# Kernel optimization log

Measured on AMD Instinct MI355X. Metric: run time of the kernel, lower is better.

The kernel has to match this reference:

```python
import jax, jax.numpy as jnp
import numpy as np

B, T, D, H, O = 64, 512, 64, 512, 64

def setup_inputs() -> dict:
    key = jax.random.key(0)
    ks = jax.random.split(key, 12)
    s = lambda fan: 1.0 / np.sqrt(fan)
    return {
        "x": jax.random.normal(ks[0], (B, T, D), jnp.float32),
        "W_ih0": jax.random.normal(ks[1], (4 * H, D), jnp.float32) * s(D),
        "W_hh0": jax.random.normal(ks[2], (4 * H, H), jnp.float32) * s(H),
        "b_ih0": jax.random.normal(ks[3], (4 * H,), jnp.float32) * s(H),
        "b_hh0": jax.random.normal(ks[4], (4 * H,), jnp.float32) * s(H),
        "W_ih1": jax.random.normal(ks[5], (4 * H, H), jnp.float32) * s(H),
        "W_hh1": jax.random.normal(ks[6], (4 * H, H), jnp.float32) * s(H),
        "b_ih1": jax.random.normal(ks[7], (4 * H,), jnp.float32) * s(H),
        "b_hh1": jax.random.normal(ks[8], (4 * H,), jnp.float32) * s(H),
        "lin_w": jax.random.normal(ks[9], (O, H), jnp.float32) * s(H),
        "lin_b": jax.random.normal(ks[10], (O,), jnp.float32) * s(H),
    }

def _lstm_layer(x_seq, h0, c0, W_ih, W_hh, b_ih, b_hh):
    # Precompute input contribution for all timesteps: [B, T, 4H]
    xg = jnp.einsum('btd,gd->btg', x_seq, W_ih) + b_ih
    def step(carry, xg_t):
        h, c = carry
        gates = xg_t + h @ W_hh.T + b_hh  # [B, 4H]
        i, f, g, o = jnp.split(gates, 4, axis=-1)
        i = jax.nn.sigmoid(i); f = jax.nn.sigmoid(f)
        g = jnp.tanh(g); o = jax.nn.sigmoid(o)
        c = f * c + i * g  # eval mode: dropout mask is identity
        h = o * jnp.tanh(c)
        return (h, c), h
    (h, c), ys = jax.lax.scan(step, (h0, c0), jnp.swapaxes(xg, 0, 1))
    return jnp.swapaxes(ys, 0, 1), h, c

def reference(x, W_ih0, W_hh0, b_ih0, b_hh0, W_ih1, W_hh1, b_ih1, b_hh1, lin_w, lin_b):
    h = jnp.zeros((x.shape[0], H), x.dtype)
    c = jnp.zeros((x.shape[0], H), x.dtype)
    # NOTE: faithful to source — h/c are only zeroed before layer 0 and
    # carried into layer 1 as its initial state.
    y0, h, c = _lstm_layer(x, h, c, W_ih0, W_hh0, b_ih0, b_hh0)
    y1, h, c = _lstm_layer(y0, h, c, W_ih1, W_hh1, b_ih1, b_hh1)
    return h @ lin_w.T + lin_b  # [B, O]
```

## Files before the change

kernel.cpp:

```cpp
#include <hip/hip_runtime.h>

#define TSEQ 512

typedef unsigned short us8v __attribute__((ext_vector_type(8)));
typedef __bf16 bf16x8 __attribute__((ext_vector_type(8)));
typedef float f32x4 __attribute__((ext_vector_type(4)));
typedef unsigned u32x4 __attribute__((ext_vector_type(4)));

#define OFF_FLAGS 0u
#define OFF_BIAS  524288u
#define OFF_X16   540672u
#define OFF_W0    4734976u
#define OFF_W1    7094272u
#define OFF_Y0    11288576u
#define OFF_RING  44843008u

static __device__ __forceinline__ unsigned short f2bf(float f) {
    unsigned u = __builtin_bit_cast(unsigned, f);
    u += 0x7fffu + ((u >> 16) & 1u);
    return (unsigned short)(u >> 16);
}
static __device__ __forceinline__ float sigmf(float x) { return 1.0f / (1.0f + __expf(-x)); }
static __device__ __forceinline__ float tanh_fast(float x) {
    float a = fabsf(x);
    float e = __expf(-2.0f * a);
    float t = (1.0f - e) / (1.0f + e);
    return copysignf(t, x);
}
static __device__ __forceinline__ f32x4 mfma16(us8v a, us8v b, f32x4 c) {
    return __builtin_amdgcn_mfma_f32_16x16x32_bf16(
        __builtin_bit_cast(bf16x8, a), __builtin_bit_cast(bf16x8, b), c, 0, 0, 0);
}

__global__ void setup_kernel(const float* __restrict__ x,
                             const float* __restrict__ wih0, const float* __restrict__ whh0,
                             const float* __restrict__ bih0, const float* __restrict__ bhh0,
                             const float* __restrict__ wih1, const float* __restrict__ whh1,
                             const float* __restrict__ bih1, const float* __restrict__ bhh1,
                             char* __restrict__ ws)
{
    unsigned idx = blockIdx.x * blockDim.x + threadIdx.x;
    unsigned stride = gridDim.x * blockDim.x;
    unsigned short* x16 = (unsigned short*)(ws + OFF_X16);
    unsigned short* w0  = (unsigned short*)(ws + OFF_W0);
    unsigned short* w1  = (unsigned short*)(ws + OFF_W1);
    float* bias = (float*)(ws + OFF_BIAS);
    const unsigned NX  = 64u*512u*64u;
    const unsigned NW0 = 2048u*576u;
    const unsigned NW1 = 2048u*1024u;
    const unsigned NT  = NX + NW0 + NW1 + 4096u;
    for (unsigned i = idx; i < NT; i += stride) {
        if (i < NX) {
            unsigned d = i & 63u, b = (i >> 6) & 63u, t = i >> 12;
            x16[i] = f2bf(x[((b << 9) + t) * 64u + d]);
        } else if (i < NX + NW0) {
            unsigned k = i - NX; unsigned r = k / 576u, c = k % 576u;
            float v = (c < 64u) ? wih0[r*64u + c] : whh0[r*512u + (c - 64u)];
            w0[k] = f2bf(v);
        } else if (i < NX + NW0 + NW1) {
            unsigned k = i - NX - NW0; unsigned r = k >> 10, c = k & 1023u;
            float v = (c < 512u) ? wih1[(r<<9) + c] : whh1[(r<<9) + (c - 512u)];
            w1[k] = f2bf(v);
        } else {
            unsigned k = i - NX - NW0 - NW1;
            float v = (k < 2048u) ? (bih0[k] + bhh0[k]) : (bih1[k-2048u] + bhh1[k-2048u]);
            bias[k] = v;
        }
    }
}

__launch_bounds__(256, 1)
__global__ void lstm_persist(char* __restrict__ ws)
{
    const int tid  = threadIdx.x;
    const int kq   = tid >> 6;
    const int lane = tid & 63;
    const int l15  = lane & 15;
    const int lhi  = lane >> 4;
    const int bg   = blockIdx.x & 3;
    const int hg   = blockIdx.x >> 2;

    unsigned* flags   = (unsigned*)(ws + OFF_FLAGS);
    const float* bias = (const float*)(ws + OFF_BIAS);
    const char*  x16  = ws + OFF_X16;
    char* y0   = ws + OFF_Y0;
    char* ring = ws + OFF_RING;

    __shared__ float gsum[64 * 68];
    __shared__ float bias_l[64];

    if (tid < 64) bias_l[tid] = bias[(tid >> 4)*512 + hg*16 + (tid & 15)];

    float cst = 0.0f;

    us8v A[4][8];
    {
        const char* w0p = ws + OFF_W0;
        #pragma unroll
        for (int m = 0; m < 4; ++m) {
            const char* base = w0p + (size_t)(m*512 + hg*16 + l15)*1152 + lhi*16;
            #pragma unroll
            for (int kk = 0; kk < 4; ++kk)
                A[m][kk] = *(const us8v*)(base + (2 + kq*4 + kk)*64);
            if (kq < 2) A[m][4] = *(const us8v*)(base + kq*64);
        }
    }
    __syncthreads();

    const int fragoff = l15*1024 + kq*256 + lhi*16;

#define POLL(WIDX) do {                                                              \
        const unsigned* fp_ = flags + (size_t)(WIDX)*128 + bg*32 + (lane & 31);      \
        unsigned fv_;                                                                \
        do {                                                                         \
            asm volatile("global_load_dword %0, %1, off sc0 sc1\n\ts_waitcnt vmcnt(0)" \
                         : "=v"(fv_) : "v"(fp_) : "memory");                         \
        } while (!__all(fv_ != 0u));                                                 \
    } while (0)

#define ACTIVATION_STORE(DSTBASE) do {                                               \
        int b_ = tid >> 4, p_ = tid & 15;                                            \
        float g4_[4];                                                                \
        _Pragma("unroll")                                                            \
        for (int g = 0; g < 4; ++g) {                                                \
            float s_ = bias_l[g*16 + p_];                                            \
            _Pragma("unroll")                                                        \
            for (int kk = 0; kk < 4; ++kk) s_ += gsum[(g*16 + p_)*68 + kk*17 + b_];  \
            g4_[g] = s_;                                                             \
        }                                                                            \
        float iv_ = sigmf(g4_[0]), fv_ = sigmf(g4_[1]);                              \
        float gv_ = tanh_fast(g4_[2]), ov_ = sigmf(g4_[3]);                          \
        cst = fv_*cst + iv_*gv_;                                                     \
        float h_ = ov_ * tanh_fast(cst);                                             \
        unsigned hv_ = f2bf(h_);                                                     \
        unsigned pk_ = (hv_ & 0xffffu) | (((unsigned)__shfl_xor((int)hv_, 1)) << 16);\
        if (!(p_ & 1)) {                                                             \
            const char* dst_ = (DSTBASE) + b_*1024 + (hg*16 + p_)*2;                 \
            asm volatile("global_store_dword %0, %1, off sc0 sc1"                    \
                         :: "v"(dst_), "v"(pk_) : "memory");                         \
        }                                                                            \
    } while (0)

    for (int t = 0; t < TSEQ; ++t) {
        us8v xf = {};
        if (kq < 2)
            xf = *(const us8v*)(x16 + (size_t)t*8192 + (bg*16 + l15)*128 + kq*64 + lhi*16);

        f32x4 acc[4] = {{0.f,0.f,0.f,0.f},{0.f,0.f,0.f,0.f},{0.f,0.f,0.f,0.f},{0.f,0.f,0.f,0.f}};
        if (t > 0) {
            POLL(t-1);
            const char* hb = y0 + ((size_t)(t-1)*4 + bg)*16384 + fragoff;
            us8v hf0 = *(const us8v*)(hb);
            us8v hf1 = *(const us8v*)(hb + 64);
            us8v hf2 = *(const us8v*)(hb + 128);
            us8v hf3 = *(const us8v*)(hb + 192);
            if (kq < 2) {
                #pragma unroll
                for (int m = 0; m < 4; ++m) acc[m] = mfma16(A[m][4], xf, acc[m]);
            }
            #pragma unroll
            for (int m = 0; m < 4; ++m) acc[m] = mfma16(A[m][0], hf0, acc[m]);
            #pragma unroll
            for (int m = 0; m < 4; ++m) acc[m] = mfma16(A[m][1], hf1, acc[m]);
            #pragma unroll
            for (int m = 0; m < 4; ++m) acc[m] = mfma16(A[m][2], hf2, acc[m]);
            #pragma unroll
            for (int m = 0; m < 4; ++m) acc[m] = mfma16(A[m][3], hf3, acc[m]);
        } else if (kq < 2) {
            #pragma unroll
            for (int m = 0; m < 4; ++m) acc[m] = mfma16(A[m][4], xf, acc[m]);
        }
        #pragma unroll
        for (int m = 0; m < 4; ++m) {
            #pragma unroll
            for (int q = 0; q < 4; ++q)
                gsum[(m*16 + lhi*4 + q)*68 + kq*17 + l15] = acc[m][q];
        }
        __syncthreads();
        ACTIVATION_STORE(y0 + ((size_t)t*4 + bg)*16384);
        asm volatile("s_waitcnt vmcnt(0)" ::: "memory");
        __syncthreads();
        if (tid == 0) {
            unsigned one = 1;
            const unsigned* fq = flags + (size_t)t*128 + bg*32 + hg;
            asm volatile("global_store_dword %0, %1, off sc0 sc1"
                         :: "v"(fq), "v"(one) : "memory");
        }
    }

    {
        const char* w1p = ws + OFF_W1;
        #pragma unroll
        for (int m = 0; m < 4; ++m) {
            const char* base = w1p + (size_t)(m*512 + hg*16 + l15)*2048 + lhi*16;
            #pragma unroll
            for (int kk = 0; kk < 4; ++kk) {
                A[m][kk]     = *(const us8v*)(base + (kq*4 + kk)*64);
                A[m][kk + 4] = *(const us8v*)(base + (16 + kq*4 + kk)*64);
            }
        }
    }
    if (tid < 64) bias_l[tid] = bias[2048 + (tid >> 4)*512 + hg*16 + (tid & 15)];
    __syncthreads();

    for (int t = 0; t < TSEQ; ++t) {
        const char* yb = y0 + ((size_t)t*4 + bg)*16384 + fragoff;
        us8v yf0 = *(const us8v*)(yb);
        us8v yf1 = *(const us8v*)(yb + 64);
        us8v yf2 = *(const us8v*)(yb + 128);
        us8v yf3 = *(const us8v*)(yb + 192);

        POLL(t == 0 ? 511 : 511 + t);

        const char* s1 = ((t == 0) ? (y0 + ((size_t)511*4 + bg)*16384)
                                   : (ring + ((size_t)((t-1) & 1)*4 + bg)*16384)) + fragoff;
        u32x4 r0, r1, r2, r3;
        {
            const char* a0 = s1;
            const char* a1 = s1 + 64;
            const char* a2 = s1 + 128;
            const char* a3 = s1 + 192;
            asm volatile("global_load_dwordx4 %0, %1, off sc0 sc1"
                         : "=v"(r0) : "v"(a0) : "memory");
            asm volatile("global_load_dwordx4 %0, %1, off sc0 sc1"
                         : "=v"(r1) : "v"(a1) : "memory");
            asm volatile("global_load_dwordx4 %0, %1, off sc0 sc1"
                         : "=v"(r2) : "v"(a2) : "memory");
            asm volatile("global_load_dwordx4 %0, %1, off sc0 sc1"
                         : "=v"(r3) : "v"(a3) : "memory");
        }

        f32x4 acc[4] = {{0.f,0.f,0.f,0.f},{0.f,0.f,0.f,0.f},{0.f,0.f,0.f,0.f},{0.f,0.f,0.f,0.f}};
        #pragma unroll
        for (int m = 0; m < 4; ++m) acc[m] = mfma16(A[m][0], yf0, acc[m]);
        #pragma unroll
        for (int m = 0; m < 4; ++m) acc[m] = mfma16(A[m][1], yf1, acc[m]);
        #pragma unroll
        for (int m = 0; m < 4; ++m) acc[m] = mfma16(A[m][2], yf2, acc[m]);
        #pragma unroll
        for (int m = 0; m < 4; ++m) acc[m] = mfma16(A[m][3], yf3, acc[m]);

        asm volatile("s_waitcnt vmcnt(0)"
                     : "+v"(r0), "+v"(r1), "+v"(r2), "+v"(r3) :: "memory");
        __builtin_amdgcn_sched_barrier(0);

        #pragma unroll
        for (int m = 0; m < 4; ++m) acc[m] = mfma16(A[m][4], __builtin_bit_cast(us8v, r0), acc[m]);
        #pragma unroll
        for (int m = 0; m < 4; ++m) acc[m] = mfma16(A[m][5], __builtin_bit_cast(us8v, r1), acc[m]);
        #pragma unroll
        for (int m = 0; m < 4; ++m) acc[m] = mfma16(A[m][6], __builtin_bit_cast(us8v, r2), acc[m]);
        #pragma unroll
        for (int m = 0; m < 4; ++m) acc[m] = mfma16(A[m][7], __builtin_bit_cast(us8v, r3), acc[m]);

        #pragma unroll
        for (int m = 0; m < 4; ++m) {
            #pragma unroll
            for (int q = 0; q < 4; ++q)
                gsum[(m*16 + lhi*4 + q)*68 + kq*17 + l15] = acc[m][q];
        }
        __syncthreads();
        ACTIVATION_STORE(ring + ((size_t)(t & 1)*4 + bg)*16384);
        asm volatile("s_waitcnt vmcnt(0)" ::: "memory");
        __syncthreads();
        if (tid == 0) {
            unsigned one = 1;
            const unsigned* fq = flags + (size_t)(512 + t)*128 + bg*32 + hg;
            asm volatile("global_store_dword %0, %1, off sc0 sc1"
                         :: "v"(fq), "v"(one) : "memory");
        }
    }
#undef POLL
#undef ACTIVATION_STORE
}

__global__ void final_linear(const char* __restrict__ ws,
                             const float* __restrict__ linw, const float* __restrict__ linb,
                             float* __restrict__ out)
{
    __shared__ float hrow[512];
    int b = blockIdx.x;
    int o = threadIdx.x;
    int bg = b >> 4, bl = b & 15;
    const char* src = ws + OFF_RING + ((size_t)1*4 + bg)*16384 + (size_t)bl*1024;
    {
        us8v v = *(const us8v*)(src + o*16);
        #pragma unroll
        for (int p = 0; p < 8; ++p)
            hrow[o*8+p] = __builtin_bit_cast(float, ((unsigned)v[p]) << 16);
    }
    __syncthreads();
    float acc = linb[o];
    const float* wrow = linw + o*512;
    #pragma unroll 8
    for (int k = 0; k < 512; ++k) acc += hrow[k] * wrow[k];
    out[b*64 + o] = acc;
}

extern "C" void kernel_launch(void* const* d_in, const int* in_sizes, int n_in,
                              void* d_out, int out_size, void* d_ws, size_t ws_size,
                              hipStream_t stream)
{
    const float* x    = (const float*)d_in[0];
    const float* wih0 = (const float*)d_in[1];
    const float* whh0 = (const float*)d_in[2];
    const float* bih0 = (const float*)d_in[3];
    const float* bhh0 = (const float*)d_in[4];
    const float* wih1 = (const float*)d_in[5];
    const float* whh1 = (const float*)d_in[6];
    const float* bih1 = (const float*)d_in[7];
    const float* bhh1 = (const float*)d_in[8];
    const float* linw = (const float*)d_in[9];
    const float* linb = (const float*)d_in[10];
    char* ws = (char*)d_ws;

    (void)hipMemsetAsync(ws + OFF_FLAGS, 0, 524288, stream);
    hipLaunchKernelGGL(setup_kernel, dim3(1024), dim3(256), 0, stream,
                       x, wih0, whh0, bih0, bhh0, wih1, whh1, bih1, bhh1, ws);
    hipLaunchKernelGGL(lstm_persist, dim3(128), dim3(256), 0, stream, ws);
    hipLaunchKernelGGL(final_linear, dim3(64), dim3(64), 0, stream,
                       ws, linw, linb, (float*)d_out);
}
```

Before: 2.603 ms.

## Replace per-step flag array with epoch counters and remove second block barrier

Per-step flag words are replaced by one epoch counter per workgroup, padded to its own 128-byte line. Consumers poll with a pipelined two-load asm loop that checks for epoch >= t. The trailing __syncthreads plus tid==0 flag store becomes an LDS atomic wave counter, so the last wave to finish publishes the epoch, and gsum is double-buffered so the next step can start without a second barrier. The hidden-state layout is also changed so each workgroup writes one contiguous 512-byte slice, with fragment loads adjusted to match. This cuts barrier and cross-workgroup signalling latency on the recurrent critical path, at the cost of subtler memory-ordering assumptions.

```diff
diff --git a/kernel.cpp b/kernel.cpp
--- a/kernel.cpp
+++ b/kernel.cpp
@@ -8,12 +8,12 @@
 typedef unsigned u32x4 __attribute__((ext_vector_type(4)));
 
 #define OFF_FLAGS 0u
-#define OFF_BIAS  524288u
-#define OFF_X16   540672u
-#define OFF_W0    4734976u
-#define OFF_W1    7094272u
-#define OFF_Y0    11288576u
-#define OFF_RING  44843008u
+#define OFF_BIAS  16384u
+#define OFF_X16   32768u
+#define OFF_W0    4227072u
+#define OFF_W1    6586368u
+#define OFF_Y0    10780672u
+#define OFF_RING  44335104u
 
 static __device__ __forceinline__ unsigned short f2bf(float f) {
     unsigned u = __builtin_bit_cast(unsigned, f);
@@ -31,6 +31,7 @@
     return __builtin_amdgcn_mfma_f32_16x16x32_bf16(
         __builtin_bit_cast(bf16x8, a), __builtin_bit_cast(bf16x8, b), c, 0, 0, 0);
 }
+static __device__ __forceinline__ us8v asb(u32x4 v) { return __builtin_bit_cast(us8v, v); }
 
 __global__ void setup_kernel(const float* __restrict__ x,
                              const float* __restrict__ wih0, const float* __restrict__ whh0,
@@ -80,15 +81,19 @@
     const int bg   = blockIdx.x & 3;
     const int hg   = blockIdx.x >> 2;
 
-    unsigned* flags   = (unsigned*)(ws + OFF_FLAGS);
     const float* bias = (const float*)(ws + OFF_BIAS);
     const char*  x16  = ws + OFF_X16;
     char* y0   = ws + OFF_Y0;
     char* ring = ws + OFF_RING;
-
-    __shared__ float gsum[64 * 68];
-    __shared__ float bias_l[64];
-
+    const char* flagbase = ws + OFF_FLAGS + bg*4096;
+    const char* fq       = flagbase + hg*128;
+
+    __shared__ __align__(16) char arena[86016];
+    float* gsum       = (float*)arena;
+    float* bias_l     = (float*)(arena + 34816);
+    unsigned* wcnt    = (unsigned*)(arena + 35072);
+
+    if (tid == 0) { wcnt[0] = 0u; wcnt[1] = 0u; }
     if (tid < 64) bias_l[tid] = bias[(tid >> 4)*512 + hg*16 + (tid & 15)];
 
     float cst = 0.0f;
@@ -107,85 +112,118 @@
     }
     __syncthreads();
 
-    const int fragoff = l15*1024 + kq*256 + lhi*16;
-
-#define POLL(WIDX) do {                                                              \
-        const unsigned* fp_ = flags + (size_t)(WIDX)*128 + bg*32 + (lane & 31);      \
-        unsigned fv_;                                                                \
-        do {                                                                         \
-            asm volatile("global_load_dword %0, %1, off sc0 sc1\n\ts_waitcnt vmcnt(0)" \
-                         : "=v"(fv_) : "v"(fp_) : "memory");                         \
-        } while (!__all(fv_ != 0u));                                                 \
+    const int base_off = kq*4096 + (lhi >> 1)*512 + l15*32 + (lhi & 1)*16;
+
+    unsigned pf0 = 0, pf1 = 0;
+
+#define POLL(EP) do {                                                            \
+        unsigned ep_ = (EP);                                                     \
+        const char* fp_ = flagbase + ((lane & 31) << 7);                         \
+        asm volatile(                                                            \
+            "global_load_dword %0, %2, off sc0 sc1\n\t"                          \
+            "global_load_dword %1, %2, off sc0 sc1\n\t"                          \
+            "1:\n\t"                                                             \
+            "s_waitcnt vmcnt(1)\n\t"                                             \
+            "v_cmp_lt_u32 vcc, %0, %3\n\t"                                       \
+            "s_cbranch_vccz 2f\n\t"                                              \
+            "global_load_dword %0, %2, off sc0 sc1\n\t"                          \
+            "s_waitcnt vmcnt(1)\n\t"                                             \
+            "v_cmp_lt_u32 vcc, %1, %3\n\t"                                       \
+            "s_cbranch_vccz 2f\n\t"                                              \
+            "global_load_dword %1, %2, off sc0 sc1\n\t"                          \
+            "s_branch 1b\n\t"                                                    \
+            "2:\n\t"                                                             \
+            : "+v"(pf0), "+v"(pf1) : "v"(fp_), "s"(ep_) : "vcc", "memory");      \
     } while (0)
 
-#define ACTIVATION_STORE(DSTBASE) do {                                               \
-        int b_ = tid >> 4, p_ = tid & 15;                                            \
-        float g4_[4];                                                                \
-        _Pragma("unroll")                                                            \
-        for (int g = 0; g < 4; ++g) {                                                \
-            float s_ = bias_l[g*16 + p_];                                            \
-            _Pragma("unroll")                                                        \
-            for (int kk = 0; kk < 4; ++kk) s_ += gsum[(g*16 + p_)*68 + kk*17 + b_];  \
-            g4_[g] = s_;                                                             \
-        }                                                                            \
-        float iv_ = sigmf(g4_[0]), fv_ = sigmf(g4_[1]);                              \
-        float gv_ = tanh_fast(g4_[2]), ov_ = sigmf(g4_[3]);                          \
-        cst = fv_*cst + iv_*gv_;                                                     \
-        float h_ = ov_ * tanh_fast(cst);                                             \
-        unsigned hv_ = f2bf(h_);                                                     \
-        unsigned pk_ = (hv_ & 0xffffu) | (((unsigned)__shfl_xor((int)hv_, 1)) << 16);\
-        if (!(p_ & 1)) {                                                             \
-            const char* dst_ = (DSTBASE) + b_*1024 + (hg*16 + p_)*2;                 \
-            asm volatile("global_store_dword %0, %1, off sc0 sc1"                    \
-                         :: "v"(dst_), "v"(pk_) : "memory");                         \
-        }                                                                            \
+#define GSUM_WRITE(PAR) do {                                                     \
+        float* gs_ = gsum + (PAR)*4352;                                          \
+        _Pragma("unroll")                                                        \
+        for (int m = 0; m < 4; ++m) {                                            \
+            _Pragma("unroll")                                                    \
+            for (int q = 0; q < 4; ++q)                                          \
+                gs_[(m*16 + lhi*4 + q)*68 + kq*17 + l15] = acc[m][q];            \
+        }                                                                        \
     } while (0)
 
+#define ACT_TAIL(SLICE, EPOCH, PAR) do {                                         \
+        int b_ = tid >> 4, p_ = tid & 15;                                        \
+        const float* gsr_ = gsum + (PAR)*4352;                                   \
+        float g4_[4];                                                            \
+        _Pragma("unroll")                                                        \
+        for (int g = 0; g < 4; ++g) {                                            \
+            float s_ = bias_l[g*16 + p_];                                        \
+            _Pragma("unroll")                                                    \
+            for (int kk = 0; kk < 4; ++kk) s_ += gsr_[(g*16 + p_)*68 + kk*17 + b_]; \
+            g4_[g] = s_;                                                         \
+        }                                                                        \
+        float iv_ = sigmf(g4_[0]), fv_ = sigmf(g4_[1]);                          \
+        float gv_ = tanh_fast(g4_[2]), ov_ = sigmf(g4_[3]);                      \
+        cst = fv_*cst + iv_*gv_;                                                 \
+        float h_ = ov_ * tanh_fast(cst);                                         \
+        unsigned hv_ = f2bf(h_);                                                 \
+        unsigned pk_ = (hv_ & 0xffffu) | (((unsigned)__shfl_xor((int)hv_, 1)) << 16); \
+        if (!(p_ & 1)) {                                                         \
+            const char* dst_ = (SLICE) + b_*32 + p_*2;                           \
+            asm volatile("global_store_dword %0, %1, off sc0 sc1"                \
+                         :: "v"(dst_), "v"(pk_) : "memory");                     \
+        }                                                                        \
+        asm volatile("s_waitcnt vmcnt(0)" ::: "memory");                         \
+        if (lane == 0) {                                                         \
+            unsigned prev_ = __hip_atomic_fetch_add(&wcnt[PAR], 1u,              \
+                                __ATOMIC_RELAXED, __HIP_MEMORY_SCOPE_WORKGROUP); \
+            if (prev_ == 3u) {                                                   \
+                __hip_atomic_store(&wcnt[PAR], 0u,                               \
+                                __ATOMIC_RELAXED, __HIP_MEMORY_SCOPE_WORKGROUP); \
+                unsigned ep_ = (EPOCH);                                          \
+                asm volatile("global_store_dword %0, %1, off sc0 sc1"            \
+                             :: "v"(fq), "v"(ep_) : "memory");                   \
+            }                                                                    \
+        }                                                                        \
+    } while (0)
+
     for (int t = 0; t < TSEQ; ++t) {
-        us8v xf = {};
-        if (kq < 2)
-            xf = *(const us8v*)(x16 + (size_t)t*8192 + (bg*16 + l15)*128 + kq*64 + lhi*16);
-
+        u32x4 xr;
+        const bool havex = (kq < 2);
+        if (havex) {
+            const char* xaddr = x16 + (size_t)t*8192 + (bg*16 + l15)*128 + kq*64 + lhi*16;
+            asm volatile("global_load_dwordx4 %0, %1, off" : "=v"(xr) : "v"(xaddr) : "memory");
+        }
         f32x4 acc[4] = {{0.f,0.f,0.f,0.f},{0.f,0.f,0.f,0.f},{0.f,0.f,0.f,0.f},{0.f,0.f,0.f,0.f}};
         if (t > 0) {
-            POLL(t-1);
-            const char* hb = y0 + ((size_t)(t-1)*4 + bg)*16384 + fragoff;
-            us8v hf0 = *(const us8v*)(hb);
-            us8v hf1 = *(const us8v*)(hb + 64);
-            us8v hf2 = *(const us8v*)(hb + 128);
-            us8v hf3 = *(const us8v*)(hb + 192);
-            if (kq < 2) {
+            POLL((unsigned)t);
+            const char* hb = y0 + ((size_t)(t-1)*4 + bg)*16384 + base_off;
+            u32x4 h0, h1, h2, h3;
+            asm volatile("global_load_dwordx4 %0, %4, off\n\t"
+                         "global_load_dwordx4 %1, %5, off\n\t"
+                         "global_load_dwordx4 %2, %6, off\n\t"
+                         "global_load_dwordx4 %3, %7, off"
+                         : "=&v"(h0), "=&v"(h1), "=&v"(h2), "=&v"(h3)
+                         : "v"(hb), "v"(hb+1024), "v"(hb+2048), "v"(hb+3072) : "memory");
+            if (havex) {
+                asm volatile("" : "+v"(xr));
                 #pragma unroll
-                for (int m = 0; m < 4; ++m) acc[m] = mfma16(A[m][4], xf, acc[m]);
+                for (int m = 0; m < 4; ++m) acc[m] = mfma16(A[m][4], asb(xr), acc[m]);
             }
-            #pragma unroll
-            for (int m = 0; m < 4; ++m) acc[m] = mfma16(A[m][0], hf0, acc[m]);
-            #pragma unroll
-            for (int m = 0; m < 4; ++m) acc[m] = mfma16(A[m][1], hf1, acc[m]);
-            #pragma unroll
-            for (int m = 0; m < 4; ++m) acc[m] = mfma16(A[m][2], hf2, acc[m]);
-            #pragma unroll
-            for (int m = 0; m < 4; ++m) acc[m] = mfma16(A[m][3], hf3, acc[m]);
-        } else if (kq < 2) {
-            #pragma unroll
-            for (int m = 0; m < 4; ++m) acc[m] = mfma16(A[m][4], xf, acc[m]);
-        }
-        #pragma unroll
-        for (int m = 0; m < 4; ++m) {
-            #pragma unroll
-            for (int q = 0; q < 4; ++q)
-                gsum[(m*16 + lhi*4 + q)*68 + kq*17 + l15] = acc[m][q];
-        }
+            asm volatile("s_waitcnt vmcnt(0)"
+                         : "+v"(h0), "+v"(h1), "+v"(h2), "+v"(h3) :: "memory");
+            asm volatile("" :: "v"(pf0), "v"(pf1));
+            #pragma unroll
+            for (int m = 0; m < 4; ++m) acc[m] = mfma16(A[m][0], asb(h0), acc[m]);
+            #pragma unroll
+            for (int m = 0; m < 4; ++m) acc[m] = mfma16(A[m][1], asb(h1), acc[m]);
+            #pragma unroll
+            for (int m = 0; m < 4; ++m) acc[m] = mfma16(A[m][2], asb(h2), acc[m]);
+            #pragma unroll
+            for (int m = 0; m < 4; ++m) acc[m] = mfma16(A[m][3], asb(h3), acc[m]);
+        } else if (havex) {
+            asm volatile("s_waitcnt vmcnt(0)" : "+v"(xr) :: "memory");
+            #pragma unroll
+            for (int m = 0; m < 4; ++m) acc[m] = mfma16(A[m][4], asb(xr), acc[m]);
+        }
+        GSUM_WRITE(t & 1);
         __syncthreads();
-        ACTIVATION_STORE(y0 + ((size_t)t*4 + bg)*16384);
-        asm volatile("s_waitcnt vmcnt(0)" ::: "memory");
-        __syncthreads();
-        if (tid == 0) {
-            unsigned one = 1;
-            const unsigned* fq = flags + (size_t)t*128 + bg*32 + hg;
-            asm volatile("global_store_dword %0, %1, off sc0 sc1"
-                         :: "v"(fq), "v"(one) : "memory");
-        }
+        ACT_TAIL(y0 + ((size_t)t*4 + bg)*16384 + hg*512, (unsigned)(t + 1), (t & 1));
     }
 
     {
@@ -204,74 +242,57 @@
     __syncthreads();
 
     for (int t = 0; t < TSEQ; ++t) {
-        const char* yb = y0 + ((size_t)t*4 + bg)*16384 + fragoff;
-        us8v yf0 = *(const us8v*)(yb);
-        us8v yf1 = *(const us8v*)(yb + 64);
-        us8v yf2 = *(const us8v*)(yb + 128);
-        us8v yf3 = *(const us8v*)(yb + 192);
-
-        POLL(t == 0 ? 511 : 511 + t);
-
-        const char* s1 = ((t == 0) ? (y0 + ((size_t)511*4 + bg)*16384)
-                                   : (ring + ((size_t)((t-1) & 1)*4 + bg)*16384)) + fragoff;
+        const char* yb = y0 + ((size_t)t*4 + bg)*16384 + base_off;
+        u32x4 yr0, yr1, yr2, yr3;
+        asm volatile("global_load_dwordx4 %0, %4, off\n\t"
+                     "global_load_dwordx4 %1, %5, off\n\t"
+                     "global_load_dwordx4 %2, %6, off\n\t"
+                     "global_load_dwordx4 %3, %7, off"
+                     : "=&v"(yr0), "=&v"(yr1), "=&v"(yr2), "=&v"(yr3)
+                     : "v"(yb), "v"(yb+1024), "v"(yb+2048), "v"(yb+3072) : "memory");
+
+        POLL((unsigned)(512 + t));
+
+        const char* rb = ((t == 0) ? (y0 + ((size_t)511*4 + bg)*16384)
+                                   : (ring + ((size_t)((t-1) & 1)*4 + bg)*16384)) + base_off;
         u32x4 r0, r1, r2, r3;
-        {
-            const char* a0 = s1;
-            const char* a1 = s1 + 64;
-            const char* a2 = s1 + 128;
-            const char* a3 = s1 + 192;
-            asm volatile("global_load_dwordx4 %0, %1, off sc0 sc1"
-                         : "=v"(r0) : "v"(a0) : "memory");
-            asm volatile("global_load_dwordx4 %0, %1, off sc0 sc1"
-                         : "=v"(r1) : "v"(a1) : "memory");
-            asm volatile("global_load_dwordx4 %0, %1, off sc0 sc1"
-                         : "=v"(r2) : "v"(a2) : "memory");
-            asm volatile("global_load_dwordx4 %0, %1, off sc0 sc1"
-                         : "=v"(r3) : "v"(a3) : "memory");
-        }
-
+        asm volatile("global_load_dwordx4 %0, %4, off sc0 sc1\n\t"
+                     "global_load_dwordx4 %1, %5, off sc0 sc1\n\t"
+                     "global_load_dwordx4 %2, %6, off sc0 sc1\n\t"
+                     "global_load_dwordx4 %3, %7, off sc0 sc1"
+                     : "=&v"(r0), "=&v"(r1), "=&v"(r2), "=&v"(r3)
+                     : "v"(rb), "v"(rb+1024), "v"(rb+2048), "v"(rb+3072) : "memory");
+
+        asm volatile("" : "+v"(yr0), "+v"(yr1), "+v"(yr2), "+v"(yr3));
         f32x4 acc[4] = {{0.f,0.f,0.f,0.f},{0.f,0.f,0.f,0.f},{0.f,0.f,0.f,0.f},{0.f,0.f,0.f,0.f}};
         #pragma unroll
-        for (int m = 0; m < 4; ++m) acc[m] = mfma16(A[m][0], yf0, acc[m]);
-        #pragma unroll
-        for (int m = 0; m < 4; ++m) acc[m] = mfma16(A[m][1], yf1, acc[m]);
-        #pragma unroll
-        for (int m = 0; m < 4; ++m) acc[m] = mfma16(A[m][2], yf2, acc[m]);
-        #pragma unroll
-        for (int m = 0; m < 4; ++m) acc[m] = mfma16(A[m][3], yf3, acc[m]);
+        for (int m = 0; m < 4; ++m) acc[m] = mfma16(A[m][0], asb(yr0), acc[m]);
+        #pragma unroll
+        for (int m = 0; m < 4; ++m) acc[m] = mfma16(A[m][1], asb(yr1), acc[m]);
+        #pragma unroll
+        for (int m = 0; m < 4; ++m) acc[m] = mfma16(A[m][2], asb(yr2), acc[m]);
+        #pragma unroll
+        for (int m = 0; m < 4; ++m) acc[m] = mfma16(A[m][3], asb(yr3), acc[m]);
 
         asm volatile("s_waitcnt vmcnt(0)"
                      : "+v"(r0), "+v"(r1), "+v"(r2), "+v"(r3) :: "memory");
-        __builtin_amdgcn_sched_barrier(0);
-
-        #pragma unroll
-        for (int m = 0; m < 4; ++m) acc[m] = mfma16(A[m][4], __builtin_bit_cast(us8v, r0), acc[m]);
-        #pragma unroll
-        for (int m = 0; m < 4; ++m) acc[m] = mfma16(A[m][5], __builtin_bit_cast(us8v, r1), acc[m]);
-        #pragma unroll
-        for (int m = 0; m < 4; ++m) acc[m] = mfma16(A[m][6], __builtin_bit_cast(us8v, r2), acc[m]);
-        #pragma unroll
-        for (int m = 0; m < 4; ++m) acc[m] = mfma16(A[m][7], __builtin_bit_cast(us8v, r3), acc[m]);
-
-        #pragma unroll
-        for (int m = 0; m < 4; ++m) {
-            #pragma unroll
-            for (int q = 0; q < 4; ++q)
-                gsum[(m*16 + lhi*4 + q)*68 + kq*17 + l15] = acc[m][q];
-        }
+        asm volatile("" :: "v"(pf0), "v"(pf1));
+        #pragma unroll
+        for (int m = 0; m < 4; ++m) acc[m] = mfma16(A[m][4], asb(r0), acc[m]);
+        #pragma unroll
+        for (int m = 0; m < 4; ++m) acc[m] = mfma16(A[m][5], asb(r1), acc[m]);
+        #pragma unroll
+        for (int m = 0; m < 4; ++m) acc[m] = mfma16(A[m][6], asb(r2), acc[m]);
+        #pragma unroll
+        for (int m = 0; m < 4; ++m) acc[m] = mfma16(A[m][7], asb(r3), acc[m]);
+
+        GSUM_WRITE(t & 1);
         __syncthreads();
-        ACTIVATION_STORE(ring + ((size_t)(t & 1)*4 + bg)*16384);
-        asm volatile("s_waitcnt vmcnt(0)" ::: "memory");
-        __syncthreads();
-        if (tid == 0) {
-            unsigned one = 1;
-            const unsigned* fq = flags + (size_t)(512 + t)*128 + bg*32 + hg;
-            asm volatile("global_store_dword %0, %1, off sc0 sc1"
-                         :: "v"(fq), "v"(one) : "memory");
-        }
+        ACT_TAIL(ring + ((size_t)(t & 1)*4 + bg)*16384 + hg*512, (unsigned)(513 + t), (t & 1));
     }
 #undef POLL
-#undef ACTIVATION_STORE
+#undef GSUM_WRITE
+#undef ACT_TAIL
 }
 
 __global__ void final_linear(const char* __restrict__ ws,
@@ -282,9 +303,10 @@
     int b = blockIdx.x;
     int o = threadIdx.x;
     int bg = b >> 4, bl = b & 15;
-    const char* src = ws + OFF_RING + ((size_t)1*4 + bg)*16384 + (size_t)bl*1024;
+    const char* src = ws + OFF_RING + ((size_t)(4 + bg))*16384
+                         + (o >> 1)*512 + bl*32 + (o & 1)*16;
     {
-        us8v v = *(const us8v*)(src + o*16);
+        us8v v = *(const us8v*)src;
         #pragma unroll
         for (int p = 0; p < 8; ++p)
             hrow[o*8+p] = __builtin_bit_cast(float, ((unsigned)v[p]) << 16);
@@ -314,7 +336,7 @@
     const float* linb = (const float*)d_in[10];
     char* ws = (char*)d_ws;
 
-    (void)hipMemsetAsync(ws + OFF_FLAGS, 0, 524288, stream);
+    (void)hipMemsetAsync(ws + OFF_FLAGS, 0, 16384, stream);
     hipLaunchKernelGGL(setup_kernel, dim3(1024), dim3(256), 0, stream,
                        x, wih0, whh0, bih0, bhh0, wih1, whh1, bih1, bhh1, ws);
     hipLaunchKernelGGL(lstm_persist, dim3(128), dim3(256), 0, stream, ws);
```

New measurement: 2.332 ms. -10.4%, faster.

## Replace per-step flag polling with epoch-tagged data packets in ring buffers

Applied to the files above, without the earlier changes.

Drops the separate flag array and the post-store barrier plus flag write. Each block now writes hidden-state fragments packed with an epoch tag into double-buffered rings, and consumers poll the data itself until every tag matches the expected step. This is meant to remove one global round trip and one __syncthreads per timestep on the serial recurrence path. The gsum LDS buffer is also double-buffered so the second barrier can go. In exchange, each tagged packet carries only half payload, so ring traffic doubles, and correctness relies on the tag lane becoming visible together with its data.

```diff
diff --git a/kernel.cpp b/kernel.cpp
--- a/kernel.cpp
+++ b/kernel.cpp
@@ -7,13 +7,14 @@
 typedef float f32x4 __attribute__((ext_vector_type(4)));
 typedef unsigned u32x4 __attribute__((ext_vector_type(4)));
 
-#define OFF_FLAGS 0u
-#define OFF_BIAS  524288u
-#define OFF_X16   540672u
-#define OFF_W0    4734976u
-#define OFF_W1    7094272u
-#define OFF_Y0    11288576u
-#define OFF_RING  44843008u
+#define OFF_BIAS  0u
+#define OFF_X16   16384u
+#define OFF_W0    4210688u
+#define OFF_W1    6569984u
+#define OFF_Y0P   10764288u
+#define OFF_RING0 44318720u
+#define OFF_RING1 44580864u
+#define OFF_HFIN  44843008u
 
 static __device__ __forceinline__ unsigned short f2bf(float f) {
     unsigned u = __builtin_bit_cast(unsigned, f);
@@ -30,6 +31,11 @@
 static __device__ __forceinline__ f32x4 mfma16(us8v a, us8v b, f32x4 c) {
     return __builtin_amdgcn_mfma_f32_16x16x32_bf16(
         __builtin_bit_cast(bf16x8, a), __builtin_bit_cast(bf16x8, b), c, 0, 0, 0);
+}
+static __device__ __forceinline__ bool fresh8(u32x4 a,u32x4 b,u32x4 c,u32x4 d,
+                                              u32x4 e,u32x4 f,u32x4 g,u32x4 h,unsigned ep) {
+    unsigned x = (a[3]^ep)|(b[3]^ep)|(c[3]^ep)|(d[3]^ep)|(e[3]^ep)|(f[3]^ep)|(g[3]^ep)|(h[3]^ep);
+    return __all((int)(x == 0u));
 }
 
 __global__ void setup_kernel(const float* __restrict__ x,
@@ -80,18 +86,20 @@
     const int bg   = blockIdx.x & 3;
     const int hg   = blockIdx.x >> 2;
 
-    unsigned* flags   = (unsigned*)(ws + OFF_FLAGS);
     const float* bias = (const float*)(ws + OFF_BIAS);
     const char*  x16  = ws + OFF_X16;
-    char* y0   = ws + OFF_Y0;
-    char* ring = ws + OFF_RING;
-
-    __shared__ float gsum[64 * 68];
-    __shared__ float bias_l[64];
+    char* y0p   = ws + OFF_Y0P;
+    char* ring0 = ws + OFF_RING0;
+    char* ring1 = ws + OFF_RING1;
+
+    __shared__ __align__(16) char arena[86016];
+    float* gsum   = (float*)arena;
+    float* bias_l = (float*)(arena + 35840);
 
     if (tid < 64) bias_l[tid] = bias[(tid >> 4)*512 + hg*16 + (tid & 15)];
 
     float cst = 0.0f;
+    const int b_ = tid >> 4, p_ = tid & 15;
 
     us8v A[4][8];
     {
@@ -107,87 +115,156 @@
     }
     __syncthreads();
 
-    const int fragoff = l15*1024 + kq*256 + lhi*16;
-
-#define POLL(WIDX) do {                                                              \
-        const unsigned* fp_ = flags + (size_t)(WIDX)*128 + bg*32 + (lane & 31);      \
-        unsigned fv_;                                                                \
-        do {                                                                         \
-            asm volatile("global_load_dword %0, %1, off sc0 sc1\n\ts_waitcnt vmcnt(0)" \
-                         : "=v"(fv_) : "v"(fp_) : "memory");                         \
-        } while (!__all(fv_ != 0u));                                                 \
+    const int vo_a   = kq*8192 + (lhi>>1)*1024 + l15*64 + (lhi&1)*32;
+    const int vo_b   = vo_a + 4096;
+    const int vo_x   = l15*128 + (kq & 1)*64 + lhi*16;
+    const int vo_y   = kq*4096 + (lhi>>1)*512 + l15*32 + (lhi&1)*16;
+    const int vo_tag = b_*64 + (p_ & 3)*16;
+    const int vo_pl  = b_*32 + (p_ & 1)*16;
+
+    u32x4 c0,c1,c2,c3,c4,c5,c6,c7;
+
+#define LOAD8(SB)                                                               \
+    asm volatile(                                                               \
+        "global_load_dwordx4 %0, %8, %10 sc0 sc1\n\t"                           \
+        "global_load_dwordx4 %1, %8, %10 offset:16 sc0 sc1\n\t"                 \
+        "global_load_dwordx4 %2, %8, %10 offset:2048 sc0 sc1\n\t"               \
+        "global_load_dwordx4 %3, %8, %10 offset:2064 sc0 sc1\n\t"               \
+        "global_load_dwordx4 %4, %9, %10 sc0 sc1\n\t"                           \
+        "global_load_dwordx4 %5, %9, %10 offset:16 sc0 sc1\n\t"                 \
+        "global_load_dwordx4 %6, %9, %10 offset:2048 sc0 sc1\n\t"               \
+        "global_load_dwordx4 %7, %9, %10 offset:2064 sc0 sc1\n\t"               \
+        "s_waitcnt vmcnt(0)"                                                    \
+        : "=&v"(c0),"=&v"(c1),"=&v"(c2),"=&v"(c3),                              \
+          "=&v"(c4),"=&v"(c5),"=&v"(c6),"=&v"(c7)                               \
+        : "v"(vo_a), "v"(vo_b), "s"(SB) : "memory")
+
+#define LOAD8X(SB, XR, SBX)                                                     \
+    asm volatile(                                                               \
+        "global_load_dwordx4 %8, %11, %12\n\t"                                  \
+        "global_load_dwordx4 %0, %9, %13 sc0 sc1\n\t"                           \
+        "global_load_dwordx4 %1, %9, %13 offset:16 sc0 sc1\n\t"                 \
+        "global_load_dwordx4 %2, %9, %13 offset:2048 sc0 sc1\n\t"               \
+        "global_load_dwordx4 %3, %9, %13 offset:2064 sc0 sc1\n\t"               \
+        "global_load_dwordx4 %4, %10, %13 sc0 sc1\n\t"                          \
+        "global_load_dwordx4 %5, %10, %13 offset:16 sc0 sc1\n\t"                \
+        "global_load_dwordx4 %6, %10, %13 offset:2048 sc0 sc1\n\t"              \
+        "global_load_dwordx4 %7, %10, %13 offset:2064 sc0 sc1\n\t"              \
+        "s_waitcnt vmcnt(0)"                                                    \
+        : "=&v"(c0),"=&v"(c1),"=&v"(c2),"=&v"(c3),                              \
+          "=&v"(c4),"=&v"(c5),"=&v"(c6),"=&v"(c7), "=&v"(XR)                    \
+        : "v"(vo_a), "v"(vo_b), "v"(vo_x), "s"(SBX), "s"(SB) : "memory")
+
+#define LOAD8Y(SB, SBY)                                                         \
+    asm volatile(                                                               \
+        "global_load_dwordx4 %8, %14, %15\n\t"                                  \
+        "global_load_dwordx4 %9, %14, %15 offset:1024\n\t"                      \
+        "global_load_dwordx4 %10, %14, %15 offset:2048\n\t"                     \
+        "global_load_dwordx4 %11, %14, %15 offset:3072\n\t"                     \
+        "global_load_dwordx4 %0, %12, %16 sc0 sc1\n\t"                          \
+        "global_load_dwordx4 %1, %12, %16 offset:16 sc0 sc1\n\t"                \
+        "global_load_dwordx4 %2, %12, %16 offset:2048 sc0 sc1\n\t"              \
+        "global_load_dwordx4 %3, %12, %16 offset:2064 sc0 sc1\n\t"              \
+        "global_load_dwordx4 %4, %13, %16 sc0 sc1\n\t"                          \
+        "global_load_dwordx4 %5, %13, %16 offset:16 sc0 sc1\n\t"                \
+        "global_load_dwordx4 %6, %13, %16 offset:2048 sc0 sc1\n\t"              \
+        "global_load_dwordx4 %7, %13, %16 offset:2064 sc0 sc1\n\t"              \
+        "s_waitcnt vmcnt(0)"                                                    \
+        : "=&v"(c0),"=&v"(c1),"=&v"(c2),"=&v"(c3),                              \
+          "=&v"(c4),"=&v"(c5),"=&v"(c6),"=&v"(c7),                              \
+          "=&v"(yr0),"=&v"(yr1),"=&v"(yr2),"=&v"(yr3)                           \
+        : "v"(vo_a), "v"(vo_b), "v"(vo_y), "s"(SBY), "s"(SB) : "memory")
+
+#define FRAG(a,b) __builtin_bit_cast(us8v, (u32x4){(a)[0],(a)[1],(b)[0],(b)[1]})
+
+#define GSUM_WRITE(PAR)                                                           \
+    do {                                                                          \
+        float* gs_ = gsum + (PAR)*4352;                                           \
+        _Pragma("unroll")                                                         \
+        for (int m = 0; m < 4; ++m) {                                             \
+            _Pragma("unroll")                                                     \
+            for (int q = 0; q < 4; ++q)                                           \
+                gs_[(m*16 + lhi*4 + q)*68 + kq*17 + l15] = acc[m][q];             \
+        }                                                                         \
     } while (0)
 
-#define ACTIVATION_STORE(DSTBASE) do {                                               \
-        int b_ = tid >> 4, p_ = tid & 15;                                            \
-        float g4_[4];                                                                \
-        _Pragma("unroll")                                                            \
-        for (int g = 0; g < 4; ++g) {                                                \
-            float s_ = bias_l[g*16 + p_];                                            \
-            _Pragma("unroll")                                                        \
-            for (int kk = 0; kk < 4; ++kk) s_ += gsum[(g*16 + p_)*68 + kk*17 + b_];  \
-            g4_[g] = s_;                                                             \
-        }                                                                            \
-        float iv_ = sigmf(g4_[0]), fv_ = sigmf(g4_[1]);                              \
-        float gv_ = tanh_fast(g4_[2]), ov_ = sigmf(g4_[3]);                          \
-        cst = fv_*cst + iv_*gv_;                                                     \
-        float h_ = ov_ * tanh_fast(cst);                                             \
-        unsigned hv_ = f2bf(h_);                                                     \
-        unsigned pk_ = (hv_ & 0xffffu) | (((unsigned)__shfl_xor((int)hv_, 1)) << 16);\
-        if (!(p_ & 1)) {                                                             \
-            const char* dst_ = (DSTBASE) + b_*1024 + (hg*16 + p_)*2;                 \
-            asm volatile("global_store_dword %0, %1, off sc0 sc1"                    \
-                         :: "v"(dst_), "v"(pk_) : "memory");                         \
-        }                                                                            \
+#define ACT_STEP(PAR, EPS, SBTAG, DOPLAIN, SBPL)                                  \
+    do {                                                                          \
+        const float* gsr = gsum + (PAR)*4352;                                     \
+        float g4[4];                                                              \
+        _Pragma("unroll")                                                         \
+        for (int g = 0; g < 4; ++g) {                                             \
+            float s = bias_l[g*16 + p_];                                          \
+            _Pragma("unroll")                                                     \
+            for (int kk = 0; kk < 4; ++kk) s += gsr[(g*16 + p_)*68 + kk*17 + b_]; \
+            g4[g] = s;                                                            \
+        }                                                                         \
+        float iv = sigmf(g4[0]), fv = sigmf(g4[1]);                               \
+        float gv = tanh_fast(g4[2]), ov = sigmf(g4[3]);                           \
+        cst = fv*cst + iv*gv;                                                     \
+        float hh = ov * tanh_fast(cst);                                           \
+        unsigned hv = f2bf(hh);                                                   \
+        unsigned pk = (hv & 0xffffu) | (((unsigned)__shfl_xor((int)hv,1)) << 16); \
+        int rbx = lane & 48;                                                      \
+        unsigned Da = (unsigned)__shfl((int)pk, rbx + (p_&3)*4);                  \
+        unsigned Db = (unsigned)__shfl((int)pk, rbx + (p_&3)*4 + 2);              \
+        unsigned P0 = (unsigned)__shfl((int)pk, rbx + (p_&1)*8);                  \
+        unsigned P1 = (unsigned)__shfl((int)pk, rbx + (p_&1)*8 + 2);              \
+        unsigned P2 = (unsigned)__shfl((int)pk, rbx + (p_&1)*8 + 4);              \
+        unsigned P3 = (unsigned)__shfl((int)pk, rbx + (p_&1)*8 + 6);              \
+        if (p_ < 4) {                                                             \
+            u32x4 tu = {Da, Db, 0u, (EPS)};                                       \
+            asm volatile("global_store_dwordx4 %0, %1, %2 sc0 sc1"                \
+                         :: "v"(vo_tag), "v"(tu), "s"(SBTAG) : "memory");         \
+        }                                                                         \
+        if ((DOPLAIN) && (p_ == 4 || p_ == 5)) {                                  \
+            u32x4 pu = {P0, P1, P2, P3};                                          \
+            asm volatile("global_store_dwordx4 %0, %1, %2 sc0 sc1"                \
+                         :: "v"(vo_pl), "v"(pu), "s"(SBPL) : "memory");           \
+        }                                                                         \
     } while (0)
 
     for (int t = 0; t < TSEQ; ++t) {
-        us8v xf = {};
-        if (kq < 2)
-            xf = *(const us8v*)(x16 + (size_t)t*8192 + (bg*16 + l15)*128 + kq*64 + lhi*16);
-
+        const int par = t & 1;
+        const char* sbx = x16 + (size_t)t*8192 + bg*2048;
+        u32x4 xr;
         f32x4 acc[4] = {{0.f,0.f,0.f,0.f},{0.f,0.f,0.f,0.f},{0.f,0.f,0.f,0.f},{0.f,0.f,0.f,0.f}};
         if (t > 0) {
-            POLL(t-1);
-            const char* hb = y0 + ((size_t)(t-1)*4 + bg)*16384 + fragoff;
-            us8v hf0 = *(const us8v*)(hb);
-            us8v hf1 = *(const us8v*)(hb + 64);
-            us8v hf2 = *(const us8v*)(hb + 128);
-            us8v hf3 = *(const us8v*)(hb + 192);
+            const char* sbr = ring0 + ((size_t)((t-1)&1)*4 + bg)*32768;
+            const unsigned ep = (unsigned)t;
+            LOAD8X(sbr, xr, sbx);
+            while (!fresh8(c0,c1,c2,c3,c4,c5,c6,c7, ep)) LOAD8(sbr);
             if (kq < 2) {
                 #pragma unroll
-                for (int m = 0; m < 4; ++m) acc[m] = mfma16(A[m][4], xf, acc[m]);
+                for (int m = 0; m < 4; ++m)
+                    acc[m] = mfma16(A[m][4], __builtin_bit_cast(us8v, xr), acc[m]);
             }
-            #pragma unroll
-            for (int m = 0; m < 4; ++m) acc[m] = mfma16(A[m][0], hf0, acc[m]);
-            #pragma unroll
-            for (int m = 0; m < 4; ++m) acc[m] = mfma16(A[m][1], hf1, acc[m]);
-            #pragma unroll
-            for (int m = 0; m < 4; ++m) acc[m] = mfma16(A[m][2], hf2, acc[m]);
-            #pragma unroll
-            for (int m = 0; m < 4; ++m) acc[m] = mfma16(A[m][3], hf3, acc[m]);
-        } else if (kq < 2) {
-            #pragma unroll
-            for (int m = 0; m < 4; ++m) acc[m] = mfma16(A[m][4], xf, acc[m]);
-        }
-        #pragma unroll
-        for (int m = 0; m < 4; ++m) {
-            #pragma unroll
-            for (int q = 0; q < 4; ++q)
-                gsum[(m*16 + lhi*4 + q)*68 + kq*17 + l15] = acc[m][q];
-        }
+            us8v h0 = FRAG(c0,c1), h1 = FRAG(c2,c3), h2 = FRAG(c4,c5), h3 = FRAG(c6,c7);
+            #pragma unroll
+            for (int m = 0; m < 4; ++m) acc[m] = mfma16(A[m][0], h0, acc[m]);
+            #pragma unroll
+            for (int m = 0; m < 4; ++m) acc[m] = mfma16(A[m][1], h1, acc[m]);
+            #pragma unroll
+            for (int m = 0; m < 4; ++m) acc[m] = mfma16(A[m][2], h2, acc[m]);
+            #pragma unroll
+            for (int m = 0; m < 4; ++m) acc[m] = mfma16(A[m][3], h3, acc[m]);
+        } else {
+            asm volatile("global_load_dwordx4 %0, %1, %2\n\ts_waitcnt vmcnt(0)"
+                         : "=&v"(xr) : "v"(vo_x), "s"(sbx) : "memory");
+            if (kq < 2) {
+                #pragma unroll
+                for (int m = 0; m < 4; ++m)
+                    acc[m] = mfma16(A[m][4], __builtin_bit_cast(us8v, xr), acc[m]);
+            }
+        }
+        GSUM_WRITE(par);
         __syncthreads();
-        ACTIVATION_STORE(y0 + ((size_t)t*4 + bg)*16384);
-        asm volatile("s_waitcnt vmcnt(0)" ::: "memory");
-        __syncthreads();
-        if (tid == 0) {
-            unsigned one = 1;
-            const unsigned* fq = flags + (size_t)t*128 + bg*32 + hg;
-            asm volatile("global_store_dword %0, %1, off sc0 sc1"
-                         :: "v"(fq), "v"(one) : "memory");
-        }
-    }
-
+        const char* sbt = ring0 + ((size_t)par*4 + bg)*32768 + hg*1024;
+        const char* sbp = y0p + ((size_t)t*4 + bg)*16384 + hg*512;
+        ACT_STEP(par, (unsigned)(t + 1), sbt, 1, sbp);
+    }
+
+    __syncthreads();
     {
         const char* w1p = ws + OFF_W1;
         #pragma unroll
@@ -204,74 +281,47 @@
     __syncthreads();
 
     for (int t = 0; t < TSEQ; ++t) {
-        const char* yb = y0 + ((size_t)t*4 + bg)*16384 + fragoff;
-        us8v yf0 = *(const us8v*)(yb);
-        us8v yf1 = *(const us8v*)(yb + 64);
-        us8v yf2 = *(const us8v*)(yb + 128);
-        us8v yf3 = *(const us8v*)(yb + 192);
-
-        POLL(t == 0 ? 511 : 511 + t);
-
-        const char* s1 = ((t == 0) ? (y0 + ((size_t)511*4 + bg)*16384)
-                                   : (ring + ((size_t)((t-1) & 1)*4 + bg)*16384)) + fragoff;
-        u32x4 r0, r1, r2, r3;
+        const int par = t & 1;
+        const char* sby = y0p + ((size_t)t*4 + bg)*16384;
+        const char* sbr = (t == 0) ? (ring0 + ((size_t)1*4 + bg)*32768)
+                                   : (ring1 + ((size_t)((t-1)&1)*4 + bg)*32768);
+        const unsigned ep = (unsigned)(512 + t);
+        u32x4 yr0, yr1, yr2, yr3;
+        LOAD8Y(sbr, sby);
+        while (!fresh8(c0,c1,c2,c3,c4,c5,c6,c7, ep)) LOAD8(sbr);
+
+        f32x4 acc[4] = {{0.f,0.f,0.f,0.f},{0.f,0.f,0.f,0.f},{0.f,0.f,0.f,0.f},{0.f,0.f,0.f,0.f}};
+        #pragma unroll
+        for (int m = 0; m < 4; ++m) acc[m] = mfma16(A[m][0], __builtin_bit_cast(us8v, yr0), acc[m]);
+        #pragma unroll
+        for (int m = 0; m < 4; ++m) acc[m] = mfma16(A[m][1], __builtin_bit_cast(us8v, yr1), acc[m]);
+        #pragma unroll
+        for (int m = 0; m < 4; ++m) acc[m] = mfma16(A[m][2], __builtin_bit_cast(us8v, yr2), acc[m]);
+        #pragma unroll
+        for (int m = 0; m < 4; ++m) acc[m] = mfma16(A[m][3], __builtin_bit_cast(us8v, yr3), acc[m]);
         {
-            const char* a0 = s1;
-            const char* a1 = s1 + 64;
-            const char* a2 = s1 + 128;
-            const char* a3 = s1 + 192;
-            asm volatile("global_load_dwordx4 %0, %1, off sc0 sc1"
-                         : "=v"(r0) : "v"(a0) : "memory");
-            asm volatile("global_load_dwordx4 %0, %1, off sc0 sc1"
-                         : "=v"(r1) : "v"(a1) : "memory");
-            asm volatile("global_load_dwordx4 %0, %1, off sc0 sc1"
-                         : "=v"(r2) : "v"(a2) : "memory");
-            asm volatile("global_load_dwordx4 %0, %1, off sc0 sc1"
-                         : "=v"(r3) : "v"(a3) : "memory");
-        }
-
-        f32x4 acc[4] = {{0.f,0.f,0.f,0.f},{0.f,0.f,0.f,0.f},{0.f,0.f,0.f,0.f},{0.f,0.f,0.f,0.f}};
-        #pragma unroll
-        for (int m = 0; m < 4; ++m) acc[m] = mfma16(A[m][0], yf0, acc[m]);
-        #pragma unroll
-        for (int m = 0; m < 4; ++m) acc[m] = mfma16(A[m][1], yf1, acc[m]);
-        #pragma unroll
-        for (int m = 0; m < 4; ++m) acc[m] = mfma16(A[m][2], yf2, acc[m]);
-        #pragma unroll
-        for (int m = 0; m < 4; ++m) acc[m] = mfma16(A[m][3], yf3, acc[m]);
-
-        asm volatile("s_waitcnt vmcnt(0)"
-                     : "+v"(r0), "+v"(r1), "+v"(r2), "+v"(r3) :: "memory");
-        __builtin_amdgcn_sched_barrier(0);
-
-        #pragma unroll
-        for (int m = 0; m < 4; ++m) acc[m] = mfma16(A[m][4], __builtin_bit_cast(us8v, r0), acc[m]);
-        #pragma unroll
-        for (int m = 0; m < 4; ++m) acc[m] = mfma16(A[m][5], __builtin_bit_cast(us8v, r1), acc[m]);
-        #pragma unroll
-        for (int m = 0; m < 4; ++m) acc[m] = mfma16(A[m][6], __builtin_bit_cast(us8v, r2), acc[m]);
-        #pragma unroll
-        for (int m = 0; m < 4; ++m) acc[m] = mfma16(A[m][7], __builtin_bit_cast(us8v, r3), acc[m]);
-
-        #pragma unroll
-        for (int m = 0; m < 4; ++m) {
-            #pragma unroll
-            for (int q = 0; q < 4; ++q)
-                gsum[(m*16 + lhi*4 + q)*68 + kq*17 + l15] = acc[m][q];
-        }
+            us8v h0 = FRAG(c0,c1), h1 = FRAG(c2,c3), h2 = FRAG(c4,c5), h3 = FRAG(c6,c7);
+            #pragma unroll
+            for (int m = 0; m < 4; ++m) acc[m] = mfma16(A[m][4], h0, acc[m]);
+            #pragma unroll
+            for (int m = 0; m < 4; ++m) acc[m] = mfma16(A[m][5], h1, acc[m]);
+            #pragma unroll
+            for (int m = 0; m < 4; ++m) acc[m] = mfma16(A[m][6], h2, acc[m]);
+            #pragma unroll
+            for (int m = 0; m < 4; ++m) acc[m] = mfma16(A[m][7], h3, acc[m]);
+        }
+        GSUM_WRITE(par);
         __syncthreads();
-        ACTIVATION_STORE(ring + ((size_t)(t & 1)*4 + bg)*16384);
-        asm volatile("s_waitcnt vmcnt(0)" ::: "memory");
-        __syncthreads();
-        if (tid == 0) {
-            unsigned one = 1;
-            const unsigned* fq = flags + (size_t)(512 + t)*128 + bg*32 + hg;
-            asm volatile("global_store_dword %0, %1, off sc0 sc1"
-                         :: "v"(fq), "v"(one) : "memory");
-        }
-    }
-#undef POLL
-#undef ACTIVATION_STORE
+        const char* sbt = ring1 + ((size_t)par*4 + bg)*32768 + hg*1024;
+        const char* sbp = ws + OFF_HFIN + ((size_t)bg*32 + hg)*512;
+        ACT_STEP(par, (unsigned)(513 + t), sbt, (t == 511), sbp);
+    }
+#undef LOAD8
+#undef LOAD8X
+#undef LOAD8Y
+#undef FRAG
+#undef GSUM_WRITE
+#undef ACT_STEP
 }
 
 __global__ void final_linear(const char* __restrict__ ws,
@@ -282,9 +332,9 @@
     int b = blockIdx.x;
     int o = threadIdx.x;
     int bg = b >> 4, bl = b & 15;
-    const char* src = ws + OFF_RING + ((size_t)1*4 + bg)*16384 + (size_t)bl*1024;
+    const char* src = ws + OFF_HFIN + ((size_t)bg*32 + (o >> 1))*512 + bl*32 + (o & 1)*16;
     {
-        us8v v = *(const us8v*)(src + o*16);
+        us8v v = *(const us8v*)src;
         #pragma unroll
         for (int p = 0; p < 8; ++p)
             hrow[o*8+p] = __builtin_bit_cast(float, ((unsigned)v[p]) << 16);
@@ -309,12 +359,13 @@
     const float* wih1 = (const float*)d_in[5];
     const float* whh1 = (const float*)d_in[6];
     const float* bih1 = (const float*)d_in[7];
+    const float* bih1_ = bih1;  (void)bih1_;
     const float* bhh1 = (const float*)d_in[8];
     const float* linw = (const float*)d_in[9];
     const float* linb = (const float*)d_in[10];
     char* ws = (char*)d_ws;
 
-    (void)hipMemsetAsync(ws + OFF_FLAGS, 0, 524288, stream);
+    (void)hipMemsetAsync(ws + OFF_RING0, 0, 262144u*2 + 65536u, stream);
     hipLaunchKernelGGL(setup_kernel, dim3(1024), dim3(256), 0, stream,
                        x, wih0, whh0, bih0, bhh0, wih1, whh1, bih1, bhh1, ws);
     hipLaunchKernelGGL(lstm_persist, dim3(128), dim3(256), 0, stream, ws);
```

New measurement: 2.489 ms. 4.4% less time.
